# Kernel optimization log

Hardware: AMD Instinct MI355X
Metric: run time of the kernel (lower is better)

## Reference

```python
import jax, jax.numpy as jnp
import numpy as np

B, L1, L, DIM_IN, DIM_H, DIM_M = 8, 64, 1024, 512, 512, 512


def setup_inputs() -> dict:
    key = jax.random.key(0)
    ks = jax.random.split(key, 7)
    return {
        "query": jax.random.normal(ks[0], (L1, DIM_H), dtype=jnp.float32),
        "keys": jax.random.normal(ks[1], (B, L, DIM_IN), dtype=jnp.float32),
        "values": jax.random.normal(ks[2], (B, L, DIM_IN), dtype=jnp.float32),
        # nn.Linear weights: Wx (dim_middle, dim_in) no bias; Wh (dim_middle, dim_h) with bias; w (dim_middle,) no bias
        "Wx": jax.random.normal(ks[3], (DIM_M, DIM_IN), dtype=jnp.float32) * 0.02,
        "Wh": jax.random.normal(ks[4], (DIM_M, DIM_H), dtype=jnp.float32) * 0.02,
        "bh": jax.random.normal(ks[5], (DIM_M,), dtype=jnp.float32) * 0.02,
        "w": jax.random.normal(ks[6], (DIM_M,), dtype=jnp.float32) * 0.02,
    }


def reference(query, keys, values, Wx, Wh, bh, w):
    # mode='concept': query [l1, dh], keys/values [b, l, d]
    kx = jnp.einsum('bld,md->blm', keys, Wx)          # [b, l, m]
    qh = jnp.einsum('qd,md->qm', query, Wh) + bh       # [l1, m]
    g = jax.nn.relu(kx[:, None, :, :] + qh[None, :, None, :])  # [b, l1, l, m]
    scores = jnp.einsum('bqlm,m->bql', g, w)           # [b, l1, l]
    e = jax.nn.softmax(scores, axis=-1)                # softmax over key len (dim 2)
    return jnp.einsum('bql,bld->bqd', e, values)       # [b, l1, dv]
```

## Files before the change

kernel.cpp:

```cpp
#include <hip/hip_runtime.h>
#include <hip/hip_bf16.h>

#define BB 8
#define L1 64
#define LL 1024
#define DD 512

typedef float f32x4 __attribute__((ext_vector_type(4)));
typedef _Float16 f16;
typedef _Float16 f16x2 __attribute__((ext_vector_type(2)));
typedef _Float16 f16x4 __attribute__((ext_vector_type(4)));
typedef _Float16 f16x8 __attribute__((ext_vector_type(8)));

union F16x8u { f16x8 v; f16x2 h[4]; };
union U4H8 { uint4 u; f16x8 v; };

__global__ __launch_bounds__(256) void kxqh_kernel(
    const float* __restrict__ keys,
    const float* __restrict__ query,
    const float* __restrict__ Wx,
    const float* __restrict__ Wh,
    const float* __restrict__ bh,
    f16* __restrict__ kx,
    f16* __restrict__ qh) {
  __shared__ char lds[32768] __attribute__((aligned(128)));
  const int t = threadIdx.x;
  const int lane = t & 63;
  const int w = t >> 6;
  const int fq = lane >> 4, fr = lane & 15;
  const int bid = blockIdx.x;

  if (bid < 8) {
    const int m0 = bid * 64;
    const int wid = w;
    f32x4 acc[4] = {};
    float4 rq[4], rw[4];
#define LOADQ(KC)                                                              \
    do {                                                                       \
      _Pragma("unroll") for (int i = 0; i < 4; ++i) {                          \
        int slot = t + i * 256;                                                \
        int row = slot >> 4, c4 = (slot & 15) * 4;                             \
        rq[i] = *reinterpret_cast<const float4*>(query + (size_t)row * DD + (KC)*64 + c4); \
        rw[i] = *reinterpret_cast<const float4*>(Wh + (size_t)(m0 + row) * DD + (KC)*64 + c4); \
      }                                                                        \
    } while (0)
    LOADQ(0);
    for (int kc = 0; kc < 8; ++kc) {
      #pragma unroll
      for (int i = 0; i < 4; ++i) {
        int slot = t + i * 256;
        int row = slot >> 4, c4 = (slot & 15) * 4;
        f16x4 hq, hw;
        hq[0] = (f16)rq[i].x; hq[1] = (f16)rq[i].y; hq[2] = (f16)rq[i].z; hq[3] = (f16)rq[i].w;
        hw[0] = (f16)rw[i].x; hw[1] = (f16)rw[i].y; hw[2] = (f16)rw[i].z; hw[3] = (f16)rw[i].w;
        *reinterpret_cast<f16x4*>(lds + row * 144 + c4 * 2) = hq;
        *reinterpret_cast<f16x4*>(lds + 9216 + row * 144 + c4 * 2) = hw;
      }
      if (kc < 7) LOADQ(kc + 1);
      __syncthreads();
      #pragma unroll
      for (int kh = 0; kh < 2; ++kh) {
        f16x8 bf = *reinterpret_cast<const f16x8*>(
            lds + 9216 + (wid * 16 + fr) * 144 + kh * 64 + fq * 16);
        #pragma unroll
        for (int qf = 0; qf < 4; ++qf) {
          f16x8 af = *reinterpret_cast<const f16x8*>(
              lds + (qf * 16 + fr) * 144 + kh * 64 + fq * 16);
          acc[qf] = __builtin_amdgcn_mfma_f32_16x16x32_f16(af, bf, acc[qf], 0, 0, 0);
        }
      }
      __syncthreads();
    }
#undef LOADQ
    #pragma unroll
    for (int qf = 0; qf < 4; ++qf) {
      int m = m0 + wid * 16 + fr;
      float bias = bh[m];
      #pragma unroll
      for (int r = 0; r < 4; ++r)
        qh[(size_t)(qf * 16 + fq * 4 + r) * DD + m] = (f16)(acc[qf][r] + bias);
    }
    return;
  }

  const int kb = bid - 8;
  const int rt = kb & 127;
  const int mt = kb >> 7;
  const int rowA0 = rt * 64;
  const int m0 = mt * 64;
  const int wr = w >> 1, wc = w & 1;

  f32x4 acc[2][2] = {};
  float4 ra[4], rb[4];

#define LOADK(K0)                                                              \
  do {                                                                         \
    _Pragma("unroll") for (int i = 0; i < 4; ++i) {                            \
      int flat = t * 4 + i * 1024;                                             \
      int row = flat >> 6, col = flat & 63;                                    \
      ra[i] = *reinterpret_cast<const float4*>(keys + (size_t)(rowA0 + row) * DD + (K0) + col); \
      rb[i] = *reinterpret_cast<const float4*>(Wx + (size_t)(m0 + row) * DD + (K0) + col); \
    }                                                                          \
  } while (0)

  LOADK(0);
  for (int s = 0; s < 8; ++s) {
    const int base = (s & 1) * 16384;
    #pragma unroll
    for (int i = 0; i < 4; ++i) {
      int flat = t * 4 + i * 1024;
      int row = flat >> 6, col = flat & 63;
      f16x4 ha, hb;
      ha[0] = (f16)ra[i].x; ha[1] = (f16)ra[i].y; ha[2] = (f16)ra[i].z; ha[3] = (f16)ra[i].w;
      hb[0] = (f16)rb[i].x; hb[1] = (f16)rb[i].y; hb[2] = (f16)rb[i].z; hb[3] = (f16)rb[i].w;
      int byte = row * 128 + ((col * 2) ^ ((row & 7) << 4));
      *reinterpret_cast<f16x4*>(lds + base + byte) = ha;
      *reinterpret_cast<f16x4*>(lds + base + 8192 + byte) = hb;
    }
    if (s < 7) LOADK((s + 1) * 64);
    __syncthreads();
    #pragma unroll
    for (int kh = 0; kh < 2; ++kh) {
      f16x8 af[2], bf[2];
      #pragma unroll
      for (int mi = 0; mi < 2; ++mi) {
        int row = wr * 32 + mi * 16 + fr;
        af[mi] = *reinterpret_cast<const f16x8*>(
            lds + base + row * 128 + ((kh * 64 + fq * 16) ^ ((row & 7) << 4)));
      }
      #pragma unroll
      for (int ni = 0; ni < 2; ++ni) {
        int row = wc * 32 + ni * 16 + fr;
        bf[ni] = *reinterpret_cast<const f16x8*>(
            lds + base + 8192 + row * 128 + ((kh * 64 + fq * 16) ^ ((row & 7) << 4)));
      }
      #pragma unroll
      for (int mi = 0; mi < 2; ++mi)
        #pragma unroll
        for (int ni = 0; ni < 2; ++ni)
          acc[mi][ni] = __builtin_amdgcn_mfma_f32_16x16x32_f16(
              af[mi], bf[ni], acc[mi][ni], 0, 0, 0);
    }
  }
#undef LOADK
  #pragma unroll
  for (int mi = 0; mi < 2; ++mi) {
    #pragma unroll
    for (int ni = 0; ni < 2; ++ni) {
      int row = rowA0 + wr * 32 + mi * 16 + fq * 4;
      int col = m0 + wc * 32 + ni * 16 + fr;
      #pragma unroll
      for (int r = 0; r < 4; ++r)
        kx[(size_t)(row + r) * DD + col] = (f16)acc[mi][ni][r];
    }
  }
}

__global__ __launch_bounds__(512) void score8_kernel(
    const f16* __restrict__ kx,
    const f16* __restrict__ qh,
    const float* __restrict__ w,
    f16* __restrict__ es,
    float* __restrict__ ssum) {
  const int b = blockIdx.x & 7;
  const int l0 = (blockIdx.x >> 3) * 32;
  const int t = threadIdx.x;
  __shared__ __align__(16) char kxs[32 * 256];
  __shared__ __align__(16) char qhs[64 * 256];
  __shared__ __align__(16) f16 wsf[DD];
  __shared__ float ssumLds[64][17];
  if (t < 128) {
    float4 wv = *reinterpret_cast<const float4*>(w + t * 4);
    f16x4 hv; hv[0] = (f16)wv.x; hv[1] = (f16)wv.y; hv[2] = (f16)wv.z; hv[3] = (f16)wv.w;
    *reinterpret_cast<f16x4*>(&wsf[t * 4]) = hv;
  }
  const int qb = t & 31;
  const int lp = t >> 5;
  float acc[2][2] = {};
  uint4 rkx, rqh[2];

#define LOADM(M0)                                                              \
  do {                                                                         \
    {                                                                          \
      int row = t >> 4, col = (t & 15) * 8;                                    \
      rkx = *reinterpret_cast<const uint4*>(kx + (size_t)(b * LL + l0 + row) * DD + (M0) + col); \
    }                                                                          \
    _Pragma("unroll") for (int p = 0; p < 2; ++p) {                            \
      int slot = t + p * 512;                                                  \
      int row = slot >> 4, col = (slot & 15) * 8;                              \
      rqh[p] = *reinterpret_cast<const uint4*>(qh + (size_t)row * DD + (M0) + col); \
    }                                                                          \
  } while (0)

  LOADM(0);
  for (int m0 = 0; m0 < DD; m0 += 128) {
    {
      int row = t >> 4, cb = (t & 15) * 16;
      *reinterpret_cast<uint4*>(kxs + row * 256 + (cb ^ ((row & 7) << 4))) = rkx;
    }
    #pragma unroll
    for (int p = 0; p < 2; ++p) {
      int slot = t + p * 512;
      int row = slot >> 4, cb = (slot & 15) * 16;
      *reinterpret_cast<uint4*>(qhs + row * 256 + (cb ^ ((row & 7) << 4))) = rqh[p];
    }
    if (m0 < DD - 128) LOADM(m0 + 128);
    __syncthreads();
    #pragma unroll 2
    for (int mm = 0; mm < 128; mm += 8) {
      const int mb = mm * 2;
      F16x8u kv0, kv1, wv;
      {
        int r0 = lp * 2, r1 = lp * 2 + 1;
        kv0.v = *reinterpret_cast<const f16x8*>(kxs + r0 * 256 + (mb ^ ((r0 & 7) << 4)));
        kv1.v = *reinterpret_cast<const f16x8*>(kxs + r1 * 256 + (mb ^ ((r1 & 7) << 4)));
      }
      wv.v = *reinterpret_cast<const f16x8*>(&wsf[m0 + mm]);
      #pragma unroll
      for (int j = 0; j < 2; ++j) {
        int qr = qb + 32 * j;
        F16x8u qv, g0, g1;
        qv.v = *reinterpret_cast<const f16x8*>(qhs + qr * 256 + (mb ^ ((qr & 7) << 4)));
        f16x8 zz = {};
        g0.v = __builtin_elementwise_max(kv0.v + qv.v, zz);
        g1.v = __builtin_elementwise_max(kv1.v + qv.v, zz);
        #pragma unroll
        for (int c = 0; c < 4; ++c) {
          acc[0][j] = __builtin_amdgcn_fdot2(g0.h[c], wv.h[c], acc[0][j], false);
          acc[1][j] = __builtin_amdgcn_fdot2(g1.h[c], wv.h[c], acc[1][j], false);
        }
      }
    }
    __syncthreads();
  }
#undef LOADM
  f16 eh[2][2];
  #pragma unroll
  for (int i = 0; i < 2; ++i)
    #pragma unroll
    for (int j = 0; j < 2; ++j)
      eh[i][j] = (f16)__expf(acc[i][j]);
  #pragma unroll
  for (int i = 0; i < 2; ++i)
    #pragma unroll
    for (int j = 0; j < 2; ++j)
      es[((size_t)b * L1 + qb + 32 * j) * LL + l0 + lp * 2 + i] = eh[i][j];
  #pragma unroll
  for (int j = 0; j < 2; ++j)
    ssumLds[qb + 32 * j][lp] = (float)eh[0][j] + (float)eh[1][j];
  __syncthreads();
  if (t < 64) {
    float S = 0.f;
    #pragma unroll
    for (int i = 0; i < 16; ++i) S += ssumLds[t][i];
    ssum[((size_t)b * L1 + t) * 32 + (l0 >> 5)] = S;
  }
}

__global__ __launch_bounds__(512) void pv3_kernel(
    const f16* __restrict__ es,
    const float* __restrict__ ssum,
    const float* __restrict__ v,
    float* __restrict__ out) {
  __shared__ __align__(16) char esl[64 * 256];
  __shared__ __align__(16) char vt[16 * 256];
  __shared__ float rowinv[64];
  __shared__ f32x4 accbuf[4][64];
  const int t = threadIdx.x;
  const int lane = t & 63;
  const int w = t >> 6;
  const int fq = lane >> 4, fr = lane & 15;
  const int bid = blockIdx.x;
  const int b = bid & 7;
  const int d0 = (bid >> 3) * 16;
  const f16* scb = es + (size_t)b * L1 * LL;
  const float* vb = v + (size_t)b * LL * DD;

  const int r0 = t >> 4;
  const int r1 = (t + 512) >> 4;
  const int ec8 = t & 15;
  const int vl = t >> 2;
  const int dq = (t & 3) * 4;
  uint4 rsc[2];
  float4 rv;

#define LOADC(LC)                                                              \
  do {                                                                         \
    rsc[0] = *reinterpret_cast<const uint4*>(scb + (size_t)r0 * LL + (LC) * 128 + ec8 * 8); \
    rsc[1] = *reinterpret_cast<const uint4*>(scb + (size_t)r1 * LL + (LC) * 128 + ec8 * 8); \
    rv = *reinterpret_cast<const float4*>(                                     \
        vb + (size_t)((LC) * 128 + vl) * DD + d0 + dq);                        \
  } while (0)

  LOADC(0);
  if (t < 64) {
    const float* pm = ssum + ((size_t)b * L1 + t) * 32;
    float S = 0.f;
    #pragma unroll
    for (int i = 0; i < 8; ++i) {
      float4 x = *reinterpret_cast<const float4*>(pm + i * 4);
      S += x.x; S += x.y; S += x.z; S += x.w;
    }
    rowinv[t] = 1.f / S;
  }
  __syncthreads();
  f32x4 acc = {};
  const int qs = (w & 3) * 16;
  const int ksh = (w >> 2) * 2;

  for (int c = 0; c < 8; ++c) {
    {
      int byte0 = r0 * 256 + ((ec8 * 16) ^ ((r0 & 7) << 4));
      *reinterpret_cast<uint4*>(esl + byte0) = rsc[0];
      int byte1 = r1 * 256 + ((ec8 * 16) ^ ((r1 & 7) << 4));
      *reinterpret_cast<uint4*>(esl + byte1) = rsc[1];
    }
    {
      float vs[4] = {rv.x, rv.y, rv.z, rv.w};
      #pragma unroll
      for (int j = 0; j < 4; ++j) {
        int d = dq + j;
        int byte = d * 256 + ((2 * vl) ^ ((d & 7) << 4));
        *reinterpret_cast<f16*>(vt + byte) = (f16)vs[j];
      }
    }
    if (c < 7) LOADC(c + 1);
    __syncthreads();
    #pragma unroll
    for (int ki = 0; ki < 2; ++ki) {
      int ks = ksh + ki;
      int qa = qs + fr;
      int colb = ks * 64 + fq * 16;
      f16x8 a = *reinterpret_cast<const f16x8*>(esl + qa * 256 + (colb ^ ((qa & 7) << 4)));
      f16x8 bb = *reinterpret_cast<const f16x8*>(vt + fr * 256 + (colb ^ ((fr & 7) << 4)));
      acc = __builtin_amdgcn_mfma_f32_16x16x32_f16(a, bb, acc, 0, 0, 0);
    }
    __syncthreads();
  }
#undef LOADC
  if (w >= 4) accbuf[w & 3][lane] = acc;
  __syncthreads();
  if (w < 4) {
    f32x4 ah = accbuf[w][lane];
    acc += ah;
    #pragma unroll
    for (int r = 0; r < 4; ++r) {
      int q = qs + fq * 4 + r;
      out[((size_t)b * L1 + q) * DD + d0 + fr] = acc[r] * rowinv[q];
    }
  }
}

extern "C" void kernel_launch(void* const* d_in, const int* in_sizes, int n_in,
                              void* d_out, int out_size, void* d_ws, size_t ws_size,
                              hipStream_t stream) {
  const float* query  = (const float*)d_in[0];
  const float* keys   = (const float*)d_in[1];
  const float* values = (const float*)d_in[2];
  const float* Wx     = (const float*)d_in[3];
  const float* Wh     = (const float*)d_in[4];
  const float* bh     = (const float*)d_in[5];
  const float* w      = (const float*)d_in[6];
  float* out = (float*)d_out;

  char* ws = (char*)d_ws;
  f16*   kx   = (f16*)ws;
  f16*   qh   = (f16*)(ws + 8388608);
  f16*   es   = (f16*)(ws + 8454144);
  float* ssum = (float*)(ws + 9502720);

  kxqh_kernel<<<1032, 256, 0, stream>>>(keys, query, Wx, Wh, bh, kx, qh);
  score8_kernel<<<256, 512, 0, stream>>>(kx, qh, w, es, ssum);
  pv3_kernel<<<256, 512, 0, stream>>>(es, ssum, values, out);
}
```

Measured before the change: 51.88 us.

## Fuse score and PV kernels into one cooperative kernel with grid sync

Merges the score/exp kernel and the probability-times-values kernel into a single cooperative launch, separated by a grid-wide barrier, with both phases sharing one LDS buffer. The aim is to drop one kernel launch and the gap between the two dependent kernels. It also widens the qh LDS swizzle from 8 to 16 rows to cut bank conflicts. The costs are the grid-sync overhead, cooperative-launch overhead, and a requirement that all 256 blocks be co-resident.

```diff
diff --git a/kernel.cpp b/kernel.cpp
--- a/kernel.cpp
+++ b/kernel.cpp
@@ -1,5 +1,8 @@
 #include <hip/hip_runtime.h>
 #include <hip/hip_bf16.h>
+#include <hip/hip_cooperative_groups.h>
+
+namespace cg = cooperative_groups;
 
 #define BB 8
 #define L1 64
@@ -156,197 +159,199 @@
   }
 }
 
-__global__ __launch_bounds__(512) void score8_kernel(
+__global__ __launch_bounds__(512) void spv_kernel(
     const f16* __restrict__ kx,
     const f16* __restrict__ qh,
     const float* __restrict__ w,
     f16* __restrict__ es,
-    float* __restrict__ ssum) {
-  const int b = blockIdx.x & 7;
-  const int l0 = (blockIdx.x >> 3) * 32;
-  const int t = threadIdx.x;
-  __shared__ __align__(16) char kxs[32 * 256];
-  __shared__ __align__(16) char qhs[64 * 256];
-  __shared__ __align__(16) f16 wsf[DD];
-  __shared__ float ssumLds[64][17];
-  if (t < 128) {
-    float4 wv = *reinterpret_cast<const float4*>(w + t * 4);
-    f16x4 hv; hv[0] = (f16)wv.x; hv[1] = (f16)wv.y; hv[2] = (f16)wv.z; hv[3] = (f16)wv.w;
-    *reinterpret_cast<f16x4*>(&wsf[t * 4]) = hv;
-  }
-  const int qb = t & 31;
-  const int lp = t >> 5;
-  float acc[2][2] = {};
-  uint4 rkx, rqh[2];
-
-#define LOADM(M0)                                                              \
-  do {                                                                         \
-    {                                                                          \
-      int row = t >> 4, col = (t & 15) * 8;                                    \
-      rkx = *reinterpret_cast<const uint4*>(kx + (size_t)(b * LL + l0 + row) * DD + (M0) + col); \
-    }                                                                          \
-    _Pragma("unroll") for (int p = 0; p < 2; ++p) {                            \
-      int slot = t + p * 512;                                                  \
-      int row = slot >> 4, col = (slot & 15) * 8;                              \
-      rqh[p] = *reinterpret_cast<const uint4*>(qh + (size_t)row * DD + (M0) + col); \
-    }                                                                          \
-  } while (0)
-
-  LOADM(0);
-  for (int m0 = 0; m0 < DD; m0 += 128) {
-    {
-      int row = t >> 4, cb = (t & 15) * 16;
-      *reinterpret_cast<uint4*>(kxs + row * 256 + (cb ^ ((row & 7) << 4))) = rkx;
-    }
-    #pragma unroll
-    for (int p = 0; p < 2; ++p) {
-      int slot = t + p * 512;
-      int row = slot >> 4, cb = (slot & 15) * 16;
-      *reinterpret_cast<uint4*>(qhs + row * 256 + (cb ^ ((row & 7) << 4))) = rqh[p];
-    }
-    if (m0 < DD - 128) LOADM(m0 + 128);
-    __syncthreads();
-    #pragma unroll 2
-    for (int mm = 0; mm < 128; mm += 8) {
-      const int mb = mm * 2;
-      F16x8u kv0, kv1, wv;
-      {
-        int r0 = lp * 2, r1 = lp * 2 + 1;
-        kv0.v = *reinterpret_cast<const f16x8*>(kxs + r0 * 256 + (mb ^ ((r0 & 7) << 4)));
-        kv1.v = *reinterpret_cast<const f16x8*>(kxs + r1 * 256 + (mb ^ ((r1 & 7) << 4)));
-      }
-      wv.v = *reinterpret_cast<const f16x8*>(&wsf[m0 + mm]);
-      #pragma unroll
-      for (int j = 0; j < 2; ++j) {
-        int qr = qb + 32 * j;
-        F16x8u qv, g0, g1;
-        qv.v = *reinterpret_cast<const f16x8*>(qhs + qr * 256 + (mb ^ ((qr & 7) << 4)));
-        f16x8 zz = {};
-        g0.v = __builtin_elementwise_max(kv0.v + qv.v, zz);
-        g1.v = __builtin_elementwise_max(kv1.v + qv.v, zz);
-        #pragma unroll
-        for (int c = 0; c < 4; ++c) {
-          acc[0][j] = __builtin_amdgcn_fdot2(g0.h[c], wv.h[c], acc[0][j], false);
-          acc[1][j] = __builtin_amdgcn_fdot2(g1.h[c], wv.h[c], acc[1][j], false);
-        }
-      }
-    }
-    __syncthreads();
-  }
-#undef LOADM
-  f16 eh[2][2];
-  #pragma unroll
-  for (int i = 0; i < 2; ++i)
-    #pragma unroll
-    for (int j = 0; j < 2; ++j)
-      eh[i][j] = (f16)__expf(acc[i][j]);
-  #pragma unroll
-  for (int i = 0; i < 2; ++i)
-    #pragma unroll
-    for (int j = 0; j < 2; ++j)
-      es[((size_t)b * L1 + qb + 32 * j) * LL + l0 + lp * 2 + i] = eh[i][j];
-  #pragma unroll
-  for (int j = 0; j < 2; ++j)
-    ssumLds[qb + 32 * j][lp] = (float)eh[0][j] + (float)eh[1][j];
-  __syncthreads();
-  if (t < 64) {
-    float S = 0.f;
-    #pragma unroll
-    for (int i = 0; i < 16; ++i) S += ssumLds[t][i];
-    ssum[((size_t)b * L1 + t) * 32 + (l0 >> 5)] = S;
-  }
-}
-
-__global__ __launch_bounds__(512) void pv3_kernel(
-    const f16* __restrict__ es,
-    const float* __restrict__ ssum,
+    float* __restrict__ ssum,
     const float* __restrict__ v,
     float* __restrict__ out) {
-  __shared__ __align__(16) char esl[64 * 256];
-  __shared__ __align__(16) char vt[16 * 256];
-  __shared__ float rowinv[64];
-  __shared__ f32x4 accbuf[4][64];
+  __shared__ __align__(16) char smem[29952];
   const int t = threadIdx.x;
-  const int lane = t & 63;
-  const int w = t >> 6;
-  const int fq = lane >> 4, fr = lane & 15;
   const int bid = blockIdx.x;
   const int b = bid & 7;
-  const int d0 = (bid >> 3) * 16;
-  const f16* scb = es + (size_t)b * L1 * LL;
-  const float* vb = v + (size_t)b * LL * DD;
-
-  const int r0 = t >> 4;
-  const int r1 = (t + 512) >> 4;
-  const int ec8 = t & 15;
-  const int vl = t >> 2;
-  const int dq = (t & 3) * 4;
-  uint4 rsc[2];
-  float4 rv;
+
+  {
+    char* kxs = smem;
+    char* qhs = smem + 8192;
+    f16* wsf = (f16*)(smem + 24576);
+    float* ssumLds = (float*)(smem + 25600);
+    const int l0 = (bid >> 3) * 32;
+    if (t < 128) {
+      float4 wv = *reinterpret_cast<const float4*>(w + t * 4);
+      f16x4 hv; hv[0] = (f16)wv.x; hv[1] = (f16)wv.y; hv[2] = (f16)wv.z; hv[3] = (f16)wv.w;
+      *reinterpret_cast<f16x4*>(wsf + t * 4) = hv;
+    }
+    const int qb = t & 31;
+    const int lp = t >> 5;
+    float acc[2][2] = {};
+    uint4 rkx, rqh[2];
+
+#define LOADM(M0)                                                              \
+    do {                                                                       \
+      {                                                                        \
+        int row = t >> 4, col = (t & 15) * 8;                                  \
+        rkx = *reinterpret_cast<const uint4*>(kx + (size_t)(b * LL + l0 + row) * DD + (M0) + col); \
+      }                                                                        \
+      _Pragma("unroll") for (int p = 0; p < 2; ++p) {                          \
+        int slot = t + p * 512;                                                \
+        int row = slot >> 4, col = (slot & 15) * 8;                            \
+        rqh[p] = *reinterpret_cast<const uint4*>(qh + (size_t)row * DD + (M0) + col); \
+      }                                                                        \
+    } while (0)
+
+    LOADM(0);
+    for (int m0 = 0; m0 < DD; m0 += 128) {
+      {
+        int row = t >> 4, cb = (t & 15) * 16;
+        *reinterpret_cast<uint4*>(kxs + row * 256 + (cb ^ ((row & 7) << 4))) = rkx;
+      }
+      #pragma unroll
+      for (int p = 0; p < 2; ++p) {
+        int slot = t + p * 512;
+        int row = slot >> 4, cb = (slot & 15) * 16;
+        *reinterpret_cast<uint4*>(qhs + row * 256 + (cb ^ ((row & 15) << 4))) = rqh[p];
+      }
+      if (m0 < DD - 128) LOADM(m0 + 128);
+      __syncthreads();
+      #pragma unroll 2
+      for (int mm = 0; mm < 128; mm += 8) {
+        const int mb = mm * 2;
+        F16x8u kv0, kv1, wv;
+        {
+          int r0 = lp * 2, r1 = lp * 2 + 1;
+          kv0.v = *reinterpret_cast<const f16x8*>(kxs + r0 * 256 + (mb ^ ((r0 & 7) << 4)));
+          kv1.v = *reinterpret_cast<const f16x8*>(kxs + r1 * 256 + (mb ^ ((r1 & 7) << 4)));
+        }
+        wv.v = *reinterpret_cast<const f16x8*>(wsf + m0 + mm);
+        #pragma unroll
+        for (int j = 0; j < 2; ++j) {
+          int qr = qb + 32 * j;
+          F16x8u qv, g0, g1;
+          qv.v = *reinterpret_cast<const f16x8*>(qhs + qr * 256 + (mb ^ ((qr & 15) << 4)));
+          f16x8 zz = {};
+          g0.v = __builtin_elementwise_max(kv0.v + qv.v, zz);
+          g1.v = __builtin_elementwise_max(kv1.v + qv.v, zz);
+          #pragma unroll
+          for (int c = 0; c < 4; ++c) {
+            acc[0][j] = __builtin_amdgcn_fdot2(g0.h[c], wv.h[c], acc[0][j], false);
+            acc[1][j] = __builtin_amdgcn_fdot2(g1.h[c], wv.h[c], acc[1][j], false);
+          }
+        }
+      }
+      __syncthreads();
+    }
+#undef LOADM
+    f16 eh[2][2];
+    #pragma unroll
+    for (int i = 0; i < 2; ++i)
+      #pragma unroll
+      for (int j = 0; j < 2; ++j)
+        eh[i][j] = (f16)__expf(acc[i][j]);
+    #pragma unroll
+    for (int i = 0; i < 2; ++i)
+      #pragma unroll
+      for (int j = 0; j < 2; ++j)
+        es[((size_t)b * L1 + qb + 32 * j) * LL + l0 + lp * 2 + i] = eh[i][j];
+    #pragma unroll
+    for (int j = 0; j < 2; ++j)
+      ssumLds[(qb + 32 * j) * 17 + lp] = (float)eh[0][j] + (float)eh[1][j];
+    __syncthreads();
+    if (t < 64) {
+      float S = 0.f;
+      #pragma unroll
+      for (int i = 0; i < 16; ++i) S += ssumLds[t * 17 + i];
+      ssum[((size_t)b * L1 + t) * 32 + (l0 >> 5)] = S;
+    }
+  }
+
+  cg::this_grid().sync();
+
+  {
+    char* esl = smem;
+    char* vt = smem + 16384;
+    float* rowinv = (float*)(smem + 20480);
+    f32x4* accbuf = (f32x4*)(smem + 20736);
+    const int lane = t & 63;
+    const int w8 = t >> 6;
+    const int fq = lane >> 4, fr = lane & 15;
+    const int d0 = (bid >> 3) * 16;
+    const f16* scb = es + (size_t)b * L1 * LL;
+    const float* vb = v + (size_t)b * LL * DD;
+
+    const int r0 = t >> 4;
+    const int r1 = (t + 512) >> 4;
+    const int ec8 = t & 15;
+    const int vl = t >> 2;
+    const int dq = (t & 3) * 4;
+    uint4 rsc[2];
+    float4 rv;
 
 #define LOADC(LC)                                                              \
-  do {                                                                         \
-    rsc[0] = *reinterpret_cast<const uint4*>(scb + (size_t)r0 * LL + (LC) * 128 + ec8 * 8); \
-    rsc[1] = *reinterpret_cast<const uint4*>(scb + (size_t)r1 * LL + (LC) * 128 + ec8 * 8); \
-    rv = *reinterpret_cast<const float4*>(                                     \
-        vb + (size_t)((LC) * 128 + vl) * DD + d0 + dq);                        \
-  } while (0)
-
-  LOADC(0);
-  if (t < 64) {
-    const float* pm = ssum + ((size_t)b * L1 + t) * 32;
-    float S = 0.f;
-    #pragma unroll
-    for (int i = 0; i < 8; ++i) {
-      float4 x = *reinterpret_cast<const float4*>(pm + i * 4);
-      S += x.x; S += x.y; S += x.z; S += x.w;
-    }
-    rowinv[t] = 1.f / S;
-  }
-  __syncthreads();
-  f32x4 acc = {};
-  const int qs = (w & 3) * 16;
-  const int ksh = (w >> 2) * 2;
-
-  for (int c = 0; c < 8; ++c) {
-    {
-      int byte0 = r0 * 256 + ((ec8 * 16) ^ ((r0 & 7) << 4));
-      *reinterpret_cast<uint4*>(esl + byte0) = rsc[0];
-      int byte1 = r1 * 256 + ((ec8 * 16) ^ ((r1 & 7) << 4));
-      *reinterpret_cast<uint4*>(esl + byte1) = rsc[1];
-    }
-    {
-      float vs[4] = {rv.x, rv.y, rv.z, rv.w};
-      #pragma unroll
-      for (int j = 0; j < 4; ++j) {
-        int d = dq + j;
-        int byte = d * 256 + ((2 * vl) ^ ((d & 7) << 4));
-        *reinterpret_cast<f16*>(vt + byte) = (f16)vs[j];
-      }
-    }
-    if (c < 7) LOADC(c + 1);
+    do {                                                                       \
+      rsc[0] = *reinterpret_cast<const uint4*>(scb + (size_t)r0 * LL + (LC) * 128 + ec8 * 8); \
+      rsc[1] = *reinterpret_cast<const uint4*>(scb + (size_t)r1 * LL + (LC) * 128 + ec8 * 8); \
+      rv = *reinterpret_cast<const float4*>(                                   \
+          vb + (size_t)((LC) * 128 + vl) * DD + d0 + dq);                      \
+    } while (0)
+
+    LOADC(0);
+    if (t < 64) {
+      const float* pm = ssum + ((size_t)b * L1 + t) * 32;
+      float S = 0.f;
+      #pragma unroll
+      for (int i = 0; i < 8; ++i) {
+        float4 x = *reinterpret_cast<const float4*>(pm + i * 4);
+        S += x.x; S += x.y; S += x.z; S += x.w;
+      }
+      rowinv[t] = 1.f / S;
+    }
     __syncthreads();
-    #pragma unroll
-    for (int ki = 0; ki < 2; ++ki) {
-      int ks = ksh + ki;
-      int qa = qs + fr;
-      int colb = ks * 64 + fq * 16;
-      f16x8 a = *reinterpret_cast<const f16x8*>(esl + qa * 256 + (colb ^ ((qa & 7) << 4)));
-      f16x8 bb = *reinterpret_cast<const f16x8*>(vt + fr * 256 + (colb ^ ((fr & 7) << 4)));
-      acc = __builtin_amdgcn_mfma_f32_16x16x32_f16(a, bb, acc, 0, 0, 0);
-    }
+    f32x4 acc = {};
+    const int qs = (w8 & 3) * 16;
+    const int ksh = (w8 >> 2) * 2;
+
+    for (int c = 0; c < 8; ++c) {
+      {
+        int byte0 = r0 * 256 + ((ec8 * 16) ^ ((r0 & 7) << 4));
+        *reinterpret_cast<uint4*>(esl + byte0) = rsc[0];
+        int byte1 = r1 * 256 + ((ec8 * 16) ^ ((r1 & 7) << 4));
+        *reinterpret_cast<uint4*>(esl + byte1) = rsc[1];
+      }
+      {
+        float vs[4] = {rv.x, rv.y, rv.z, rv.w};
+        #pragma unroll
+        for (int j = 0; j < 4; ++j) {
+          int d = dq + j;
+          int byte = d * 256 + ((2 * vl) ^ ((d & 7) << 4));
+          *reinterpret_cast<f16*>(vt + byte) = (f16)vs[j];
+        }
+      }
+      if (c < 7) LOADC(c + 1);
+      __syncthreads();
+      #pragma unroll
+      for (int ki = 0; ki < 2; ++ki) {
+        int ks = ksh + ki;
+        int qa = qs + fr;
+        int colb = ks * 64 + fq * 16;
+        f16x8 a = *reinterpret_cast<const f16x8*>(esl + qa * 256 + (colb ^ ((qa & 7) << 4)));
+        f16x8 bb = *reinterpret_cast<const f16x8*>(vt + fr * 256 + (colb ^ ((fr & 7) << 4)));
+        acc = __builtin_amdgcn_mfma_f32_16x16x32_f16(a, bb, acc, 0, 0, 0);
+      }
+      __syncthreads();
+    }
+#undef LOADC
+    if (w8 >= 4) accbuf[(w8 & 3) * 64 + lane] = acc;
     __syncthreads();
-  }
-#undef LOADC
-  if (w >= 4) accbuf[w & 3][lane] = acc;
-  __syncthreads();
-  if (w < 4) {
-    f32x4 ah = accbuf[w][lane];
-    acc += ah;
-    #pragma unroll
-    for (int r = 0; r < 4; ++r) {
-      int q = qs + fq * 4 + r;
-      out[((size_t)b * L1 + q) * DD + d0 + fr] = acc[r] * rowinv[q];
+    if (w8 < 4) {
+      f32x4 ah = accbuf[w8 * 64 + lane];
+      acc += ah;
+      #pragma unroll
+      for (int r = 0; r < 4; ++r) {
+        int q = qs + fq * 4 + r;
+        out[((size_t)b * L1 + q) * DD + d0 + fr] = acc[r] * rowinv[q];
+      }
     }
   }
 }
@@ -370,6 +375,10 @@
   float* ssum = (float*)(ws + 9502720);
 
   kxqh_kernel<<<1032, 256, 0, stream>>>(keys, query, Wx, Wh, bh, kx, qh);
-  score8_kernel<<<256, 512, 0, stream>>>(kx, qh, w, es, ssum);
-  pv3_kernel<<<256, 512, 0, stream>>>(es, ssum, values, out);
+
+  const f16* kxc = kx; const f16* qhc = qh; const float* wc = w;
+  f16* esc = es; float* ssc = ssum; const float* vc = values; float* oc = out;
+  void* args[7] = {&kxc, &qhc, &wc, &esc, &ssc, &vc, &oc};
+  hipLaunchCooperativeKernel((const void*)spv_kernel, dim3(256), dim3(512),
+                             args, 0u, stream);
 }
```

New measurement: 93.68 us. +80.6%, slower.
